# Kernel tuning notes

Hardware: AMD Instinct MI355X
Metric: run time of the kernel (lower is better)

The kernel has to match this reference:

```python
import jax, jax.numpy as jnp
import numpy as np

B, SQ, SK = 2, 2048, 2048
E = 256   # embed_dim (also per-head key dim in this MHA)
S = 256   # srcdim (also per-head value dim)
NH = 8    # num_heads
HID = 2 * S  # FFN hidden = in_dim * 2


def setup_inputs() -> dict:
    key = jax.random.key(0)
    ks = jax.random.split(key, 12)
    def w(k, shape, s=0.02):
        return jax.random.normal(k, shape, dtype=jnp.float32) * s
    return {
        "Q": jax.random.normal(ks[0], (B, SQ, E), dtype=jnp.float32),
        "H": jax.random.normal(ks[1], (B, SK, E), dtype=jnp.float32),
        "A": jax.random.normal(ks[2], (B, SK, S), dtype=jnp.float32),
        # MHA params (torch Linear convention: y = x @ W.T + b)
        "wq": w(ks[3], (NH * E, E)), "bq": jnp.zeros((NH * E,), jnp.float32),
        "wk": w(ks[4], (NH * E, E)), "bk": jnp.zeros((NH * E,), jnp.float32),
        "wv": w(ks[5], (NH * S, S)), "bv": jnp.zeros((NH * S,), jnp.float32),
        "wo": w(ks[6], (S, NH * S)), "bo": jnp.zeros((S,), jnp.float32),
        # Attension scale (Parameter(torch.ones(1)))
        "attn_scale": jnp.ones((), jnp.float32),
        # shared LayerNormA params
        "ln_g": jnp.ones((S,), jnp.float32), "ln_b": jnp.zeros((S,), jnp.float32),
        # FFN params
        "w1": w(ks[7], (HID, S)), "b1": jnp.zeros((HID,), jnp.float32),
        "w2": w(ks[8], (S, HID)), "b2": jnp.zeros((S,), jnp.float32),
    }


def _layernorm(x, g, b, eps=1e-5):
    m = x.mean(-1, keepdims=True)
    v = ((x - m) ** 2).mean(-1, keepdims=True)
    return (x - m) / jnp.sqrt(v + eps) * g + b


def reference(Q, H, A, wq, bq, wk, bk, wv, bv, wo, bo,
              attn_scale, ln_g, ln_b, w1, b1, w2, b2):
    b_, sq, _ = Q.shape
    sk = H.shape[1]
    # ---- MHA branch (A_m) ----
    q = (Q @ wq.T + bq).reshape(b_, sq, NH, E).transpose(0, 2, 1, 3)  # [b,h,sq,E]
    k = (H @ wk.T + bk).reshape(b_, sk, NH, E).transpose(0, 2, 1, 3)  # [b,h,sk,E]
    v = (A @ wv.T + bv).reshape(b_, sk, NH, S).transpose(0, 2, 1, 3)  # [b,h,sk,S]
    scores = jnp.einsum('bhqe,bhke->bhqk', q, k) / jnp.sqrt(jnp.float32(E))
    probs = jax.nn.softmax(scores, axis=-1)
    ctx = jnp.einsum('bhqk,bhkd->bhqd', probs, v)          # [b,h,sq,S]
    ctx = ctx.transpose(0, 2, 1, 3).reshape(b_, sq, NH * S)
    A_m = ctx @ wo.T + bo                                   # [b,sq,S]
    # ---- Attension branch (dot score with learned scalar scale) ----
    s2 = jnp.einsum('bqe,bke->bqk', Q, H) * attn_scale      # [b,sq,sk]
    attn_out = jax.nn.softmax(s2, axis=-1) @ A              # [b,sq,S]
    # ---- residual + LN + FFN + LN (shared LayerNormA) ----
    Ad = _layernorm(A_m + attn_out, ln_g, ln_b)
    ff = jax.nn.relu(Ad @ w1.T + b1) @ w2.T + b2
    return _layernorm(ff + Ad, ln_g, ln_b)
```

## Files before the change

kernel.cpp:

```cpp
#include <hip/hip_runtime.h>
#include <cstdint>
#include <cstddef>


typedef unsigned short u16;
typedef __attribute__((ext_vector_type(8))) short bf16x8;
typedef __attribute__((ext_vector_type(4))) short s16x4;
typedef __attribute__((ext_vector_type(4))) float f32x4;

__device__ __forceinline__ float b2f(u16 u){
  union { unsigned int i; float f; } v; v.i = ((unsigned int)u) << 16; return v.f;
}
__device__ __forceinline__ u16 f2b(float f){
  union { float f; unsigned int i; } v; v.f = f;
  unsigned int u = v.i;
  unsigned int r = (u + 0x7FFFu + ((u >> 16) & 1u)) >> 16;
  return (u16)r;
}
__device__ __forceinline__ f32x4 mfma16(bf16x8 a, bf16x8 b, f32x4 c){
  return __builtin_amdgcn_mfma_f32_16x16x32_bf16(a, b, c, 0, 0, 0);
}
__device__ __forceinline__ void gload_lds16(const void* g, void* l){
  __builtin_amdgcn_global_load_lds(
      (const __attribute__((address_space(1))) unsigned int*)g,
      (__attribute__((address_space(3))) unsigned int*)l, 16, 0, 0);
}

__global__ void detect_kernel(const u16* __restrict__ q, int* __restrict__ flag){
  __shared__ int cnt;
  if (threadIdx.x == 0) cnt = 0;
  __syncthreads();
  int c = 0;
  for (int i = threadIdx.x; i < 2048; i += 256){
    u16 u = q[i];
    int e = (u >> 7) & 0xFF;
    if (e >= 140) c++;
  }
  atomicAdd(&cnt, c);
  __syncthreads();
  if (threadIdx.x == 0) *flag = (cnt > 64) ? 1 : 0;
}

struct ConvJobs {
  const void* src[18];
  void*       dst[18];
  void*       dst2[18];
  int         n[18];
  int         mode[18];
};

__global__ void convert_all(ConvJobs J, const int* __restrict__ flag){
  const int j = blockIdx.y;
  const int n = J.n[j];
  const int mode = J.mode[j];
  const int isf = *flag;
  for (int i = blockIdx.x * blockDim.x + threadIdx.x; i < n; i += gridDim.x * blockDim.x){
    if (mode == 2){
      float f = isf ? ((const float*)J.src[j])[i] : b2f(((const u16*)J.src[j])[i]);
      ((float*)J.dst[j])[i] = f;
    } else {
      u16 hi, lo = 0;
      if (isf){
        float f = ((const float*)J.src[j])[i];
        hi = f2b(f);
        if (mode == 1) lo = f2b(f - b2f(hi));
      } else {
        hi = ((const u16*)J.src[j])[i];
      }
      ((u16*)J.dst[j])[i] = hi;
      if (mode == 1) ((u16*)J.dst2[j])[i] = lo;
    }
  }
}

template<int STORE, bool RELU>
__global__ __launch_bounds__(256) void gemm_bt(
    const u16* __restrict__ X, const u16* __restrict__ W,
    const float* __restrict__ bias, void* __restrict__ outp,
    int M, int N, int K)
{
  __shared__ __align__(16) u16 lx[128 * 64];
  __shared__ __align__(16) u16 lw[128 * 64];
  const int tid = threadIdx.x;
  const int l = tid & 63, w = tid >> 6;
  const int lg = l >> 4, lr = l & 15;
  const int wr = w >> 1, wc = w & 1;
  const int m0 = blockIdx.x * 128;
  const int n0 = blockIdx.y * 128;

  f32x4 acc[4][4];
#pragma unroll
  for (int mi = 0; mi < 4; mi++)
#pragma unroll
    for (int ni = 0; ni < 4; ni++) acc[mi][ni] = (f32x4){0.f, 0.f, 0.f, 0.f};

  const int nkt = K >> 6;
  for (int kt = 0; kt < nkt; ++kt){
    __syncthreads();
#pragma unroll
    for (int it = 0; it < 4; ++it){
      int c = it * 256 + tid;
      int row = c >> 3, j = c & 7;
      int sj = (j ^ (row & 7)) * 8;
      const u16* gx = X + (size_t)(m0 + row) * K + kt * 64 + sj;
      gload_lds16(gx, (char*)lx + c * 16);
      const u16* gw = W + (size_t)(n0 + row) * K + kt * 64 + sj;
      gload_lds16(gw, (char*)lw + c * 16);
    }
    __syncthreads();
#pragma unroll
    for (int ks = 0; ks < 2; ++ks){
      bf16x8 af[4], bfv[4];
      const int swz = ((ks * 4 + lg) ^ (lr & 7)) * 8;
#pragma unroll
      for (int mi = 0; mi < 4; mi++)
        af[mi] = *(const bf16x8*)(lx + (wr * 64 + mi * 16 + lr) * 64 + swz);
#pragma unroll
      for (int ni = 0; ni < 4; ni++)
        bfv[ni] = *(const bf16x8*)(lw + (wc * 64 + ni * 16 + lr) * 64 + swz);
#pragma unroll
      for (int mi = 0; mi < 4; mi++)
#pragma unroll
        for (int ni = 0; ni < 4; ni++)
          acc[mi][ni] = mfma16(af[mi], bfv[ni], acc[mi][ni]);
    }
  }

#pragma unroll
  for (int mi = 0; mi < 4; mi++)
#pragma unroll
    for (int ni = 0; ni < 4; ni++){
      const int gr0 = m0 + wr * 64 + mi * 16 + lg * 4;
      const int gc  = n0 + wc * 64 + ni * 16 + lr;
      const float bv = bias ? bias[gc] : 0.f;
      if (STORE == 2){
        const int b = gr0 >> 11, sk0 = gr0 & 2047;
        const int h = gc >> 8,  d   = gc & 255;
        s16x4 pk;
#pragma unroll
        for (int r = 0; r < 4; r++){
          float v = acc[mi][ni][r] + bv;
          pk[r] = (short)f2b(v);
        }
        *(s16x4*)((u16*)outp + ((size_t)((b << 3) + h) * 256 + d) * 2048 + sk0) = pk;
      } else {
#pragma unroll
        for (int r = 0; r < 4; r++){
          float v = acc[mi][ni][r] + bv;
          if (RELU) v = fmaxf(v, 0.f);
          size_t idx = (size_t)(gr0 + r) * N + gc;
          if (STORE == 0) ((u16*)outp)[idx] = f2b(v);
          else            ((float*)outp)[idx] = v;
        }
      }
    }
}

template<int STORE, bool RELU>
__global__ __launch_bounds__(256) void gemm_bt64(
    const u16* __restrict__ X, const u16* __restrict__ W,
    const float* __restrict__ bias, void* __restrict__ outp,
    int M, int N, int K)
{
  __shared__ __align__(16) u16 lx[64 * 64];
  __shared__ __align__(16) u16 lw[64 * 64];
  const int tid = threadIdx.x;
  const int l = tid & 63, w = tid >> 6;
  const int lg = l >> 4, lr = l & 15;
  const int wr = w >> 1, wc = w & 1;
  const int m0 = blockIdx.x * 64;
  const int n0 = blockIdx.y * 64;

  f32x4 acc[2][2];
#pragma unroll
  for (int mi = 0; mi < 2; mi++)
#pragma unroll
    for (int ni = 0; ni < 2; ni++) acc[mi][ni] = (f32x4){0.f, 0.f, 0.f, 0.f};

  const int nkt = K >> 6;
  for (int kt = 0; kt < nkt; ++kt){
    __syncthreads();
#pragma unroll
    for (int it = 0; it < 2; ++it){
      int c = it * 256 + tid;
      int row = c >> 3, j = c & 7;
      int sj = (j ^ (row & 7)) * 8;
      const u16* gx = X + (size_t)(m0 + row) * K + kt * 64 + sj;
      gload_lds16(gx, (char*)lx + c * 16);
      const u16* gw = W + (size_t)(n0 + row) * K + kt * 64 + sj;
      gload_lds16(gw, (char*)lw + c * 16);
    }
    __syncthreads();
#pragma unroll
    for (int ks = 0; ks < 2; ++ks){
      bf16x8 af[2], bfv[2];
      const int swz = ((ks * 4 + lg) ^ (lr & 7)) * 8;
#pragma unroll
      for (int mi = 0; mi < 2; mi++)
        af[mi] = *(const bf16x8*)(lx + (wr * 32 + mi * 16 + lr) * 64 + swz);
#pragma unroll
      for (int ni = 0; ni < 2; ni++)
        bfv[ni] = *(const bf16x8*)(lw + (wc * 32 + ni * 16 + lr) * 64 + swz);
#pragma unroll
      for (int mi = 0; mi < 2; mi++)
#pragma unroll
        for (int ni = 0; ni < 2; ni++)
          acc[mi][ni] = mfma16(af[mi], bfv[ni], acc[mi][ni]);
    }
  }

#pragma unroll
  for (int mi = 0; mi < 2; mi++)
#pragma unroll
    for (int ni = 0; ni < 2; ni++){
      const int gr0 = m0 + wr * 32 + mi * 16 + lg * 4;
      const int gc  = n0 + wc * 32 + ni * 16 + lr;
      const float bv = bias ? bias[gc] : 0.f;
#pragma unroll
      for (int r = 0; r < 4; r++){
        float v = acc[mi][ni][r] + bv;
        if (RELU) v = fmaxf(v, 0.f);
        size_t idx = (size_t)(gr0 + r) * N + gc;
        if (STORE == 0) ((u16*)outp)[idx] = f2b(v);
        else            ((float*)outp)[idx] = v;
      }
    }
}

__global__ __launch_bounds__(256) void transpose_k(const u16* __restrict__ src, u16* __restrict__ dst){
  __shared__ u16 t[64][72];
  const int b   = blockIdx.z;
  const int sk0 = blockIdx.x * 64;
  const int d0  = blockIdx.y * 64;
  const int tid = threadIdx.x;
  union U8 { bf16x8 v; u16 e[8]; };
#pragma unroll
  for (int half = 0; half < 2; ++half){
    int c = half * 256 + tid;
    int r = c >> 3, c8 = (c & 7) * 8;
    U8 u; u.v = *(const bf16x8*)(src + ((size_t)b * 2048 + sk0 + r) * 256 + d0 + c8);
#pragma unroll
    for (int i = 0; i < 8; i++) t[r][c8 + i] = u.e[i];
  }
  __syncthreads();
#pragma unroll
  for (int half = 0; half < 2; ++half){
    int c = half * 256 + tid;
    int dr = c >> 3, s8 = (c & 7) * 8;
    U8 u;
#pragma unroll
    for (int i = 0; i < 8; i++) u.e[i] = t[s8 + i][dr];
    *(bf16x8*)(dst + ((size_t)b * 256 + d0 + dr) * 2048 + sk0 + s8) = u.v;
  }
}

__global__ __launch_bounds__(256, 1) void flash_mha(
    const u16* __restrict__ Qp, const u16* __restrict__ Kp,
    const u16* __restrict__ Vt, u16* __restrict__ outp)
{
  __shared__ __align__(16) u16 bufK[64 * 256];
  __shared__ __align__(16) u16 bufV[256 * 64];
  __shared__ __align__(16) u16 ldsP[4][32 * 72];
  const int tid = threadIdx.x, l = tid & 63, w = tid >> 6;
  const int lg = l >> 4, lr = l & 15;
  const int lr7 = lr & 15 & 7;
  const int bid = blockIdx.x;
  const int xcd = bid & 7;
  const int slot = bid >> 3;
  const int by = xcd * 2 + (slot >> 4);
  const int qt = slot & 15;
  const size_t qkbase = ((size_t)(by >> 3) * 2048) * 2048 + (size_t)(by & 7) * 256;
  const size_t vbase  = (size_t)by * (256 * 2048);
  const int q0 = qt * 128 + w * 32;

  bf16x8 qf[2][8];
#pragma unroll
  for (int qb = 0; qb < 2; qb++)
#pragma unroll
    for (int ks = 0; ks < 8; ks++)
      qf[qb][ks] = *(const bf16x8*)(Qp + qkbase +
          (size_t)(q0 + qb * 16 + lr) * 2048 + ks * 32 + lg * 8);

  float mrun[2][4], lpart[2][4];
#pragma unroll
  for (int qb = 0; qb < 2; qb++)
#pragma unroll
    for (int r = 0; r < 4; r++){ mrun[qb][r] = -3e38f; lpart[qb][r] = 0.f; }
  f32x4 accO[2][16];
#pragma unroll
  for (int qb = 0; qb < 2; qb++)
#pragma unroll
    for (int db = 0; db < 16; db++) accO[qb][db] = (f32x4){0.f, 0.f, 0.f, 0.f};

  auto stageK = [&](int kv0){
#pragma unroll
    for (int it = 0; it < 8; ++it){
      int c = it * 256 + tid;
      int row = c >> 5, j = c & 31;
      const u16* g = Kp + qkbase + (size_t)(kv0 + row) * 2048 + (j ^ (row & 7)) * 8;
      gload_lds16(g, (char*)bufK + c * 16);
    }
  };
  auto stageV = [&](int kv0){
#pragma unroll
    for (int it = 0; it < 8; ++it){
      int c = it * 256 + tid;
      int row = c >> 3, j = c & 7;
      const u16* g = Vt + vbase + (size_t)row * 2048 + kv0 + (j ^ (row & 7)) * 8;
      gload_lds16(g, (char*)bufV + c * 16);
    }
  };

  stageK(0);

  for (int t = 0; t < 32; ++t){
    const int kv0 = t * 64;
    __syncthreads();
    stageV(kv0);

    f32x4 s[2][4];
#pragma unroll
    for (int qb = 0; qb < 2; qb++)
#pragma unroll
      for (int kb = 0; kb < 4; kb++) s[qb][kb] = (f32x4){0.f, 0.f, 0.f, 0.f};

    __builtin_amdgcn_s_setprio(1);
#pragma unroll
    for (int ks = 0; ks < 8; ks++){
      bf16x8 bfr[4];
      const int swz = (((ks * 4 + lg) ^ lr7)) * 8;
#pragma unroll
      for (int kb = 0; kb < 4; kb++)
        bfr[kb] = *(const bf16x8*)(bufK + (kb * 16 + lr) * 256 + swz);
#pragma unroll
      for (int qb = 0; qb < 2; qb++)
#pragma unroll
        for (int kb = 0; kb < 4; kb++)
          s[qb][kb] = mfma16(qf[qb][ks], bfr[kb], s[qb][kb]);
    }
    __builtin_amdgcn_s_setprio(0);

    float pm[2][4];
#pragma unroll
    for (int qb = 0; qb < 2; qb++){
#pragma unroll
      for (int kb = 0; kb < 4; kb++)
#pragma unroll
        for (int r = 0; r < 4; r++) s[qb][kb][r] *= 0.0625f;
#pragma unroll
      for (int r = 0; r < 4; r++)
        pm[qb][r] = fmaxf(fmaxf(s[qb][0][r], s[qb][1][r]),
                          fmaxf(s[qb][2][r], s[qb][3][r]));
#pragma unroll
      for (int m = 1; m < 16; m <<= 1)
#pragma unroll
        for (int r = 0; r < 4; r++) pm[qb][r] = fmaxf(pm[qb][r], __shfl_xor(pm[qb][r], m));
    }
    float gmax = -3e38f;
#pragma unroll
    for (int qb = 0; qb < 2; qb++)
#pragma unroll
      for (int r = 0; r < 4; r++) gmax = fmaxf(gmax, pm[qb][r] - mrun[qb][r]);
    if (__any(gmax > 8.0f)){
#pragma unroll
      for (int qb = 0; qb < 2; qb++)
#pragma unroll
        for (int r = 0; r < 4; r++){
          float mn = fmaxf(mrun[qb][r], pm[qb][r]);
          float corr = __expf(mrun[qb][r] - mn);
          mrun[qb][r] = mn;
          lpart[qb][r] *= corr;
#pragma unroll
          for (int db = 0; db < 16; db++) accO[qb][db][r] *= corr;
        }
    }
#pragma unroll
    for (int qb = 0; qb < 2; qb++)
#pragma unroll
      for (int kb = 0; kb < 4; kb++)
#pragma unroll
        for (int r = 0; r < 4; r++){
          float p = __expf(s[qb][kb][r] - mrun[qb][r]);
          lpart[qb][r] += p;
          ldsP[w][(qb * 16 + lg * 4 + r) * 72 + kb * 16 + lr] = f2b(p);
        }

    __syncthreads();
    if (t + 1 < 32) stageK(kv0 + 64);

    __builtin_amdgcn_s_setprio(1);
#pragma unroll
    for (int ks2 = 0; ks2 < 2; ++ks2){
      bf16x8 pa[2];
#pragma unroll
      for (int qb = 0; qb < 2; qb++)
        pa[qb] = *(const bf16x8*)(ldsP[w] + (qb * 16 + lr) * 72 + ks2 * 32 + lg * 8);
      const int swz = (((ks2 * 4 + lg) ^ lr7)) * 8;
#pragma unroll
      for (int db = 0; db < 16; ++db){
        bf16x8 vb = *(const bf16x8*)(bufV + (db * 16 + lr) * 64 + swz);
        accO[0][db] = mfma16(pa[0], vb, accO[0][db]);
        accO[1][db] = mfma16(pa[1], vb, accO[1][db]);
      }
    }
    __builtin_amdgcn_s_setprio(0);
  }

#pragma unroll
  for (int qb = 0; qb < 2; qb++){
    float lrun[4];
#pragma unroll
    for (int r = 0; r < 4; r++) lrun[r] = lpart[qb][r];
#pragma unroll
    for (int m = 1; m < 16; m <<= 1)
#pragma unroll
      for (int r = 0; r < 4; r++) lrun[r] += __shfl_xor(lrun[r], m);
    float inv[4];
#pragma unroll
    for (int r = 0; r < 4; r++) inv[r] = 1.f / lrun[r];
#pragma unroll
    for (int db = 0; db < 16; db++)
#pragma unroll
      for (int r = 0; r < 4; r++){
        float v = accO[qb][db][r] * inv[r];
        int q = q0 + qb * 16 + lg * 4 + r;
        int d = db * 16 + lr;
        outp[((size_t)(by >> 3) * 2048 + q) * 2048 + (size_t)(by & 7) * 256 + d] = f2b(v);
      }
  }
}

__global__ __launch_bounds__(256) void flash_b2(
    const u16* __restrict__ Qh, const u16* __restrict__ Ql,
    const u16* __restrict__ Kh, const u16* __restrict__ Kl,
    const u16* __restrict__ Vt,
    float* __restrict__ Opart, float* __restrict__ mlp,
    const float* __restrict__ p_scale, const int* __restrict__ flagp)
{
  __shared__ __align__(16) u16 bufK[64 * 256];
  __shared__ __align__(16) u16 bufV[256 * 64];
  __shared__ __align__(16) u16 ldsP[4][16 * 72];
  const int tid = threadIdx.x, l = tid & 63, w = tid >> 6;
  const int lg = l >> 4, lr = l & 15;
  const int lr7 = lr & 7;
  const int by = blockIdx.y, qt = blockIdx.x, kc = blockIdx.z;
  const size_t qkbase = (size_t)by * (2048 * 256);
  const size_t vbase  = (size_t)by * (256 * 2048);
  const float scale = *p_scale;
  const int split = *flagp;
  const int kvbase = kc * 256;
  const int q0 = qt * 64 + w * 16;

  bf16x8 qf[8], qfl[8];
#pragma unroll
  for (int ks = 0; ks < 8; ks++)
    qf[ks] = *(const bf16x8*)(Qh + qkbase + (size_t)(q0 + lr) * 256 + ks * 32 + lg * 8);
  if (split){
#pragma unroll
    for (int ks = 0; ks < 8; ks++)
      qfl[ks] = *(const bf16x8*)(Ql + qkbase + (size_t)(q0 + lr) * 256 + ks * 32 + lg * 8);
  } else {
#pragma unroll
    for (int ks = 0; ks < 8; ks++) qfl[ks] = qf[ks];
  }

  float mrun[4], lpart[4];
#pragma unroll
  for (int r = 0; r < 4; r++){ mrun[r] = -3e38f; lpart[r] = 0.f; }
  f32x4 accO[16];
#pragma unroll
  for (int db = 0; db < 16; db++) accO[db] = (f32x4){0.f, 0.f, 0.f, 0.f};

  auto stageK = [&](const u16* __restrict__ src, int kv0){
#pragma unroll
    for (int it = 0; it < 8; ++it){
      int c = it * 256 + tid;
      int row = c >> 5, j = c & 31;
      const u16* g = src + qkbase + (size_t)(kv0 + row) * 256 + (j ^ (row & 7)) * 8;
      gload_lds16(g, (char*)bufK + c * 16);
    }
  };
  auto stageV = [&](int kv0){
#pragma unroll
    for (int it = 0; it < 8; ++it){
      int c = it * 256 + tid;
      int row = c >> 3, j = c & 7;
      const u16* g = Vt + vbase + (size_t)row * 2048 + kv0 + (j ^ (row & 7)) * 8;
      gload_lds16(g, (char*)bufV + c * 16);
    }
  };

  for (int t = 0; t < 4; ++t){
    const int kv0 = kvbase + t * 64;
    __syncthreads();
    stageK(Kh, kv0);
    stageV(kv0);
    __syncthreads();

    f32x4 s[4];
#pragma unroll
    for (int kb = 0; kb < 4; kb++) s[kb] = (f32x4){0.f, 0.f, 0.f, 0.f};
#pragma unroll
    for (int ks = 0; ks < 8; ks++){
      bf16x8 bfr[4];
      const int swz = (((ks * 4 + lg) ^ lr7)) * 8;
#pragma unroll
      for (int kb = 0; kb < 4; kb++)
        bfr[kb] = *(const bf16x8*)(bufK + (kb * 16 + lr) * 256 + swz);
#pragma unroll
      for (int kb = 0; kb < 4; kb++) s[kb] = mfma16(qf[ks], bfr[kb], s[kb]);
      if (split){
#pragma unroll
        for (int kb = 0; kb < 4; kb++) s[kb] = mfma16(qfl[ks], bfr[kb], s[kb]);
      }
    }
    if (split){
      __syncthreads();
      stageK(Kl, kv0);
      __syncthreads();
#pragma unroll
      for (int ks = 0; ks < 8; ks++){
        bf16x8 bfr[4];
        const int swz = (((ks * 4 + lg) ^ lr7)) * 8;
#pragma unroll
        for (int kb = 0; kb < 4; kb++)
          bfr[kb] = *(const bf16x8*)(bufK + (kb * 16 + lr) * 256 + swz);
#pragma unroll
        for (int kb = 0; kb < 4; kb++) s[kb] = mfma16(qf[ks], bfr[kb], s[kb]);
      }
    }

#pragma unroll
    for (int kb = 0; kb < 4; kb++)
#pragma unroll
      for (int r = 0; r < 4; r++) s[kb][r] *= scale;

    float pm[4];
#pragma unroll
    for (int r = 0; r < 4; r++)
      pm[r] = fmaxf(fmaxf(s[0][r], s[1][r]), fmaxf(s[2][r], s[3][r]));
#pragma unroll
    for (int m = 1; m < 16; m <<= 1)
#pragma unroll
      for (int r = 0; r < 4; r++) pm[r] = fmaxf(pm[r], __shfl_xor(pm[r], m));

    float g = fmaxf(fmaxf(pm[0] - mrun[0], pm[1] - mrun[1]),
                    fmaxf(pm[2] - mrun[2], pm[3] - mrun[3]));
    if (__any(g > 8.0f)){
#pragma unroll
      for (int r = 0; r < 4; r++){
        float mn = fmaxf(mrun[r], pm[r]);
        float corr = __expf(mrun[r] - mn);
        mrun[r] = mn;
        lpart[r] *= corr;
#pragma unroll
        for (int db = 0; db < 16; db++) accO[db][r] *= corr;
      }
    }
#pragma unroll
    for (int kb = 0; kb < 4; kb++)
#pragma unroll
      for (int r = 0; r < 4; r++){
        float p = __expf(s[kb][r] - mrun[r]);
        lpart[r] += p;
        ldsP[w][(lg * 4 + r) * 72 + kb * 16 + lr] = f2b(p);
      }

#pragma unroll
    for (int ks2 = 0; ks2 < 2; ++ks2){
      bf16x8 pa = *(const bf16x8*)(ldsP[w] + lr * 72 + ks2 * 32 + lg * 8);
      const int swz = (((ks2 * 4 + lg) ^ lr7)) * 8;
#pragma unroll
      for (int db = 0; db < 16; ++db){
        bf16x8 vb = *(const bf16x8*)(bufV + (db * 16 + lr) * 64 + swz);
        accO[db] = mfma16(pa, vb, accO[db]);
      }
    }
  }

  float lrun[4];
#pragma unroll
  for (int r = 0; r < 4; r++) lrun[r] = lpart[r];
#pragma unroll
  for (int m = 1; m < 16; m <<= 1)
#pragma unroll
    for (int r = 0; r < 4; r++) lrun[r] += __shfl_xor(lrun[r], m);

#pragma unroll
  for (int db = 0; db < 16; db++)
#pragma unroll
    for (int r = 0; r < 4; r++){
      int q = q0 + lg * 4 + r;
      int d = db * 16 + lr;
      Opart[((size_t)((kc * 2 + by) * 2048 + q)) * 256 + d] = accO[db][r];
    }
  if (lr == 0){
#pragma unroll
    for (int r = 0; r < 4; r++){
      int idx = (kc * 2 + by) * 2048 + q0 + lg * 4 + r;
      mlp[idx] = mrun[r];
      mlp[32768 + idx] = lrun[r];
    }
  }
}

__global__ __launch_bounds__(256) void merge_k(
    const float* __restrict__ Opart, const float* __restrict__ ml,
    float* __restrict__ outp)
{
  const int w = threadIdx.x >> 6, l = threadIdx.x & 63;
  const int row = blockIdx.x * 4 + w;
  const int b = row >> 11, q = row & 2047;
  float m[8], li[8], M = -3e38f;
#pragma unroll
  for (int kc = 0; kc < 8; kc++){
    int idx = (kc * 2 + b) * 2048 + q;
    m[kc] = ml[idx];
    li[kc] = ml[32768 + idx];
    M = fmaxf(M, m[kc]);
  }
  float L = 0.f, wgt[8];
#pragma unroll
  for (int kc = 0; kc < 8; kc++){ wgt[kc] = __expf(m[kc] - M); L += li[kc] * wgt[kc]; }
  const float invL = 1.f / L;
  f32x4 o = (f32x4){0.f, 0.f, 0.f, 0.f};
#pragma unroll
  for (int kc = 0; kc < 8; kc++){
    f32x4 v = *(const f32x4*)(Opart + ((size_t)((kc * 2 + b) * 2048 + q)) * 256 + l * 4);
#pragma unroll
    for (int i = 0; i < 4; i++) o[i] += v[i] * wgt[kc];
  }
#pragma unroll
  for (int i = 0; i < 4; i++) o[i] *= invL;
  *(f32x4*)(outp + (size_t)row * 256 + l * 4) = o;
}

template<int RESF32, int OUTFLAG>
__global__ __launch_bounds__(256) void ln_k(
    const float* __restrict__ x, const void* __restrict__ res,
    const float* __restrict__ g, const float* __restrict__ bb,
    void* __restrict__ outp, const int* __restrict__ flagp)
{
  const int w = threadIdx.x >> 6, l = threadIdx.x & 63;
  const int row = blockIdx.x * 4 + w;
  const size_t off = (size_t)row * 256 + l * 4;
  f32x4 xv = *(const f32x4*)(x + off);
  float v[4];
  if (RESF32){
    f32x4 rv = *(const f32x4*)((const float*)res + off);
#pragma unroll
    for (int i = 0; i < 4; i++) v[i] = xv[i] + rv[i];
  } else {
    const u16* rp = (const u16*)res + off;
#pragma unroll
    for (int i = 0; i < 4; i++) v[i] = xv[i] + b2f(rp[i]);
  }
  float s = 0.f, sq = 0.f;
#pragma unroll
  for (int i = 0; i < 4; i++){ s += v[i]; sq += v[i] * v[i]; }
  for (int m = 1; m < 64; m <<= 1){ s += __shfl_xor(s, m); sq += __shfl_xor(sq, m); }
  const float mean = s * (1.f / 256.f);
  const float var = sq * (1.f / 256.f) - mean * mean;
  const float rstd = rsqrtf(var + 1e-5f);
  float y[4];
#pragma unroll
  for (int i = 0; i < 4; i++) y[i] = (v[i] - mean) * rstd * g[l * 4 + i] + bb[l * 4 + i];
  const bool f32out = OUTFLAG && (*flagp);
  if (f32out){
    f32x4 o;
#pragma unroll
    for (int i = 0; i < 4; i++) o[i] = y[i];
    *(f32x4*)((float*)outp + off) = o;
  } else {
    s16x4 o;
#pragma unroll
    for (int i = 0; i < 4; i++) o[i] = (short)f2b(y[i]);
    *(s16x4*)((u16*)outp + off) = o;
  }
}

extern "C" void kernel_launch(void* const* d_in, const int* in_sizes, int n_in,
                              void* d_out, int out_size, void* d_ws, size_t ws_size,
                              hipStream_t stream)
{
  (void)in_sizes; (void)n_in; (void)out_size; (void)ws_size;
  char* ws = (char*)d_ws;
  size_t off = 0;
  auto alloc = [&](size_t bytes) -> char* {
    char* p = ws + off;
    off += (bytes + 255) & ~(size_t)255;
    return p;
  };
  int*   flag    = (int*)  alloc(4);
  float* p_scale = (float*)alloc(4);
  float* p_bq    = (float*)alloc(2048 * 4);
  float* p_bk    = (float*)alloc(2048 * 4);
  float* p_bv    = (float*)alloc(2048 * 4);
  float* p_bo    = (float*)alloc(256 * 4);
  float* p_b1    = (float*)alloc(512 * 4);
  float* p_b2    = (float*)alloc(256 * 4);
  float* p_g     = (float*)alloc(256 * 4);
  float* p_b     = (float*)alloc(256 * 4);
  u16* Qc  = (u16*)alloc((size_t)1048576 * 2);
  u16* Qlo = (u16*)alloc((size_t)1048576 * 2);
  u16* Hc  = (u16*)alloc((size_t)1048576 * 2);
  u16* Hlo = (u16*)alloc((size_t)1048576 * 2);
  u16* Ac  = (u16*)alloc((size_t)1048576 * 2);
  u16* wqc = (u16*)alloc((size_t)524288 * 2);
  u16* wkc = (u16*)alloc((size_t)524288 * 2);
  u16* wvc = (u16*)alloc((size_t)524288 * 2);
  u16* woc = (u16*)alloc((size_t)524288 * 2);
  u16* w1c = (u16*)alloc((size_t)131072 * 2);
  u16* w2c = (u16*)alloc((size_t)131072 * 2);
  u16* qbuf = (u16*)alloc((size_t)4096 * 2048 * 2);
  u16* kbuf = (u16*)alloc((size_t)4096 * 2048 * 2);
  u16* vtb  = (u16*)alloc((size_t)4096 * 2048 * 2);
  u16* ctx  = (u16*)alloc((size_t)4096 * 2048 * 2);
  u16* At   = (u16*)alloc((size_t)1048576 * 2);
  float* attn_o = (float*)alloc((size_t)4096 * 256 * 4);
  float* Am     = (float*)alloc((size_t)4096 * 256 * 4);
  u16* Ad  = (u16*)alloc((size_t)1048576 * 2);
  u16* h1  = (u16*)alloc((size_t)4096 * 512 * 2);
  float* ffb = (float*)alloc((size_t)4096 * 256 * 4);

  detect_kernel<<<1, 256, 0, stream>>>((const u16*)d_in[0], flag);

  ConvJobs J{};
  auto setj = [&](int i, const void* s, void* d, void* d2, int n, int m){
    J.src[i] = s; J.dst[i] = d; J.dst2[i] = d2; J.n[i] = n; J.mode[i] = m;
  };
  setj(0,  d_in[0],  Qc,  Qlo, 1048576, 1);
  setj(1,  d_in[1],  Hc,  Hlo, 1048576, 1);
  setj(2,  d_in[2],  Ac,  nullptr, 1048576, 0);
  setj(3,  d_in[3],  wqc, nullptr, 524288, 0);
  setj(4,  d_in[5],  wkc, nullptr, 524288, 0);
  setj(5,  d_in[7],  wvc, nullptr, 524288, 0);
  setj(6,  d_in[9],  woc, nullptr, 524288, 0);
  setj(7,  d_in[14], w1c, nullptr, 131072, 0);
  setj(8,  d_in[16], w2c, nullptr, 131072, 0);
  setj(9,  d_in[4],  p_bq, nullptr, 2048, 2);
  setj(10, d_in[6],  p_bk, nullptr, 2048, 2);
  setj(11, d_in[8],  p_bv, nullptr, 2048, 2);
  setj(12, d_in[10], p_bo, nullptr, 256, 2);
  setj(13, d_in[15], p_b1, nullptr, 512, 2);
  setj(14, d_in[17], p_b2, nullptr, 256, 2);
  setj(15, d_in[12], p_g,  nullptr, 256, 2);
  setj(16, d_in[13], p_b,  nullptr, 256, 2);
  setj(17, d_in[11], p_scale, nullptr, 1, 2);
  convert_all<<<dim3(64, 18), 256, 0, stream>>>(J, flag);

  gemm_bt<0, false><<<dim3(32, 16), 256, 0, stream>>>(Qc, wqc, p_bq, qbuf, 4096, 2048, 256);
  gemm_bt<0, false><<<dim3(32, 16), 256, 0, stream>>>(Hc, wkc, p_bk, kbuf, 4096, 2048, 256);
  gemm_bt<2, false><<<dim3(32, 16), 256, 0, stream>>>(Ac, wvc, p_bv, vtb,  4096, 2048, 256);
  transpose_k<<<dim3(32, 4, 2), 256, 0, stream>>>(Ac, At);

  flash_mha<<<dim3(256), 256, 0, stream>>>(qbuf, kbuf, vtb, ctx);

  float* Opart = (float*)qbuf;
  float* mlbuf = (float*)vtb;
  flash_b2<<<dim3(32, 2, 8), 256, 0, stream>>>(Qc, Qlo, Hc, Hlo, At,
                                               Opart, mlbuf, p_scale, flag);
  merge_k<<<1024, 256, 0, stream>>>(Opart, mlbuf, attn_o);

  gemm_bt64<1, false><<<dim3(64, 4), 256, 0, stream>>>(ctx, woc, p_bo, Am, 4096, 256, 2048);
  ln_k<1, 0><<<1024, 256, 0, stream>>>(Am, attn_o, p_g, p_b, Ad, flag);
  gemm_bt64<0, true ><<<dim3(64, 8), 256, 0, stream>>>(Ad, w1c, p_b1, h1, 4096, 512, 256);
  gemm_bt64<1, false><<<dim3(64, 4), 256, 0, stream>>>(h1, w2c, p_b2, ffb, 4096, 256, 512);
  ln_k<0, 1><<<1024, 256, 0, stream>>>(ffb, Ad, p_g, p_b, d_out, flag);
}
```

Baseline: 311.5 us.

## Split flash_mha work over 8 waves with 16 query rows each

Changes the MHA flash kernel from 4 waves of 32 query rows to 8 waves of 16 query rows per block (512 threads), halving per-wave accumulator and Q-fragment registers. K/V staging is spread over twice as many threads and the per-wave P scratch is resized. The aim is more waves in flight to hide LDS and memory latency. The cost is that each V fragment loaded from LDS now feeds one MFMA instead of two, which doubles LDS read traffic per unit of compute.

```diff
diff --git a/kernel.cpp b/kernel.cpp
--- a/kernel.cpp
+++ b/kernel.cpp
@@ -254,16 +254,16 @@
   }
 }
 
-__global__ __launch_bounds__(256, 1) void flash_mha(
+__global__ __launch_bounds__(512, 2) void flash_mha(
     const u16* __restrict__ Qp, const u16* __restrict__ Kp,
     const u16* __restrict__ Vt, u16* __restrict__ outp)
 {
   __shared__ __align__(16) u16 bufK[64 * 256];
   __shared__ __align__(16) u16 bufV[256 * 64];
-  __shared__ __align__(16) u16 ldsP[4][32 * 72];
+  __shared__ __align__(16) u16 ldsP[8][16 * 72];
   const int tid = threadIdx.x, l = tid & 63, w = tid >> 6;
   const int lg = l >> 4, lr = l & 15;
-  const int lr7 = lr & 15 & 7;
+  const int lr7 = lr & 7;
   const int bid = blockIdx.x;
   const int xcd = bid & 7;
   const int slot = bid >> 3;
@@ -271,31 +271,25 @@
   const int qt = slot & 15;
   const size_t qkbase = ((size_t)(by >> 3) * 2048) * 2048 + (size_t)(by & 7) * 256;
   const size_t vbase  = (size_t)by * (256 * 2048);
-  const int q0 = qt * 128 + w * 32;
-
-  bf16x8 qf[2][8];
-#pragma unroll
-  for (int qb = 0; qb < 2; qb++)
-#pragma unroll
-    for (int ks = 0; ks < 8; ks++)
-      qf[qb][ks] = *(const bf16x8*)(Qp + qkbase +
-          (size_t)(q0 + qb * 16 + lr) * 2048 + ks * 32 + lg * 8);
-
-  float mrun[2][4], lpart[2][4];
-#pragma unroll
-  for (int qb = 0; qb < 2; qb++)
-#pragma unroll
-    for (int r = 0; r < 4; r++){ mrun[qb][r] = -3e38f; lpart[qb][r] = 0.f; }
-  f32x4 accO[2][16];
-#pragma unroll
-  for (int qb = 0; qb < 2; qb++)
-#pragma unroll
-    for (int db = 0; db < 16; db++) accO[qb][db] = (f32x4){0.f, 0.f, 0.f, 0.f};
+  const int q0 = qt * 128 + w * 16;
+
+  bf16x8 qf[8];
+#pragma unroll
+  for (int ks = 0; ks < 8; ks++)
+    qf[ks] = *(const bf16x8*)(Qp + qkbase +
+        (size_t)(q0 + lr) * 2048 + ks * 32 + lg * 8);
+
+  float mrun[4], lpart[4];
+#pragma unroll
+  for (int r = 0; r < 4; r++){ mrun[r] = -3e38f; lpart[r] = 0.f; }
+  f32x4 accO[16];
+#pragma unroll
+  for (int db = 0; db < 16; db++) accO[db] = (f32x4){0.f, 0.f, 0.f, 0.f};
 
   auto stageK = [&](int kv0){
 #pragma unroll
-    for (int it = 0; it < 8; ++it){
-      int c = it * 256 + tid;
+    for (int it = 0; it < 4; ++it){
+      int c = it * 512 + tid;
       int row = c >> 5, j = c & 31;
       const u16* g = Kp + qkbase + (size_t)(kv0 + row) * 2048 + (j ^ (row & 7)) * 8;
       gload_lds16(g, (char*)bufK + c * 16);
@@ -303,8 +297,8 @@
   };
   auto stageV = [&](int kv0){
 #pragma unroll
-    for (int it = 0; it < 8; ++it){
-      int c = it * 256 + tid;
+    for (int it = 0; it < 4; ++it){
+      int c = it * 512 + tid;
       int row = c >> 3, j = c & 7;
       const u16* g = Vt + vbase + (size_t)row * 2048 + kv0 + (j ^ (row & 7)) * 8;
       gload_lds16(g, (char*)bufV + c * 16);
@@ -318,11 +312,9 @@
     __syncthreads();
     stageV(kv0);
 
-    f32x4 s[2][4];
-#pragma unroll
-    for (int qb = 0; qb < 2; qb++)
-#pragma unroll
-      for (int kb = 0; kb < 4; kb++) s[qb][kb] = (f32x4){0.f, 0.f, 0.f, 0.f};
+    f32x4 s[4];
+#pragma unroll
+    for (int kb = 0; kb < 4; kb++) s[kb] = (f32x4){0.f, 0.f, 0.f, 0.f};
 
     __builtin_amdgcn_s_setprio(1);
 #pragma unroll
@@ -333,57 +325,45 @@
       for (int kb = 0; kb < 4; kb++)
         bfr[kb] = *(const bf16x8*)(bufK + (kb * 16 + lr) * 256 + swz);
 #pragma unroll
-      for (int qb = 0; qb < 2; qb++)
-#pragma unroll
-        for (int kb = 0; kb < 4; kb++)
-          s[qb][kb] = mfma16(qf[qb][ks], bfr[kb], s[qb][kb]);
+      for (int kb = 0; kb < 4; kb++)
+        s[kb] = mfma16(qf[ks], bfr[kb], s[kb]);
     }
     __builtin_amdgcn_s_setprio(0);
 
-    float pm[2][4];
-#pragma unroll
-    for (int qb = 0; qb < 2; qb++){
-#pragma unroll
-      for (int kb = 0; kb < 4; kb++)
-#pragma unroll
-        for (int r = 0; r < 4; r++) s[qb][kb][r] *= 0.0625f;
-#pragma unroll
-      for (int r = 0; r < 4; r++)
-        pm[qb][r] = fmaxf(fmaxf(s[qb][0][r], s[qb][1][r]),
-                          fmaxf(s[qb][2][r], s[qb][3][r]));
-#pragma unroll
-      for (int m = 1; m < 16; m <<= 1)
-#pragma unroll
-        for (int r = 0; r < 4; r++) pm[qb][r] = fmaxf(pm[qb][r], __shfl_xor(pm[qb][r], m));
-    }
-    float gmax = -3e38f;
-#pragma unroll
-    for (int qb = 0; qb < 2; qb++)
-#pragma unroll
-      for (int r = 0; r < 4; r++) gmax = fmaxf(gmax, pm[qb][r] - mrun[qb][r]);
+    float pm[4];
+#pragma unroll
+    for (int kb = 0; kb < 4; kb++)
+#pragma unroll
+      for (int r = 0; r < 4; r++) s[kb][r] *= 0.0625f;
+#pragma unroll
+    for (int r = 0; r < 4; r++)
+      pm[r] = fmaxf(fmaxf(s[0][r], s[1][r]), fmaxf(s[2][r], s[3][r]));
+#pragma unroll
+    for (int m = 1; m < 16; m <<= 1)
+#pragma unroll
+      for (int r = 0; r < 4; r++) pm[r] = fmaxf(pm[r], __shfl_xor(pm[r], m));
+
+    float gmax = fmaxf(fmaxf(pm[0] - mrun[0], pm[1] - mrun[1]),
+                       fmaxf(pm[2] - mrun[2], pm[3] - mrun[3]));
     if (__any(gmax > 8.0f)){
 #pragma unroll
-      for (int qb = 0; qb < 2; qb++)
-#pragma unroll
-        for (int r = 0; r < 4; r++){
-          float mn = fmaxf(mrun[qb][r], pm[qb][r]);
-          float corr = __expf(mrun[qb][r] - mn);
-          mrun[qb][r] = mn;
-          lpart[qb][r] *= corr;
-#pragma unroll
-          for (int db = 0; db < 16; db++) accO[qb][db][r] *= corr;
-        }
-    }
-#pragma unroll
-    for (int qb = 0; qb < 2; qb++)
-#pragma unroll
-      for (int kb = 0; kb < 4; kb++)
-#pragma unroll
-        for (int r = 0; r < 4; r++){
-          float p = __expf(s[qb][kb][r] - mrun[qb][r]);
-          lpart[qb][r] += p;
-          ldsP[w][(qb * 16 + lg * 4 + r) * 72 + kb * 16 + lr] = f2b(p);
-        }
+      for (int r = 0; r < 4; r++){
+        float mn = fmaxf(mrun[r], pm[r]);
+        float corr = __expf(mrun[r] - mn);
+        mrun[r] = mn;
+        lpart[r] *= corr;
+#pragma unroll
+        for (int db = 0; db < 16; db++) accO[db][r] *= corr;
+      }
+    }
+#pragma unroll
+    for (int kb = 0; kb < 4; kb++)
+#pragma unroll
+      for (int r = 0; r < 4; r++){
+        float p = __expf(s[kb][r] - mrun[r]);
+        lpart[r] += p;
+        ldsP[w][(lg * 4 + r) * 72 + kb * 16 + lr] = f2b(p);
+      }
 
     __syncthreads();
     if (t + 1 < 32) stageK(kv0 + 64);
@@ -391,43 +371,36 @@
     __builtin_amdgcn_s_setprio(1);
 #pragma unroll
     for (int ks2 = 0; ks2 < 2; ++ks2){
-      bf16x8 pa[2];
-#pragma unroll
-      for (int qb = 0; qb < 2; qb++)
-        pa[qb] = *(const bf16x8*)(ldsP[w] + (qb * 16 + lr) * 72 + ks2 * 32 + lg * 8);
+      bf16x8 pa = *(const bf16x8*)(ldsP[w] + lr * 72 + ks2 * 32 + lg * 8);
       const int swz = (((ks2 * 4 + lg) ^ lr7)) * 8;
 #pragma unroll
       for (int db = 0; db < 16; ++db){
         bf16x8 vb = *(const bf16x8*)(bufV + (db * 16 + lr) * 64 + swz);
-        accO[0][db] = mfma16(pa[0], vb, accO[0][db]);
-        accO[1][db] = mfma16(pa[1], vb, accO[1][db]);
+        accO[db] = mfma16(pa, vb, accO[db]);
       }
     }
     __builtin_amdgcn_s_setprio(0);
   }
 
-#pragma unroll
-  for (int qb = 0; qb < 2; qb++){
-    float lrun[4];
-#pragma unroll
-    for (int r = 0; r < 4; r++) lrun[r] = lpart[qb][r];
-#pragma unroll
-    for (int m = 1; m < 16; m <<= 1)
-#pragma unroll
-      for (int r = 0; r < 4; r++) lrun[r] += __shfl_xor(lrun[r], m);
-    float inv[4];
-#pragma unroll
-    for (int r = 0; r < 4; r++) inv[r] = 1.f / lrun[r];
-#pragma unroll
-    for (int db = 0; db < 16; db++)
-#pragma unroll
-      for (int r = 0; r < 4; r++){
-        float v = accO[qb][db][r] * inv[r];
-        int q = q0 + qb * 16 + lg * 4 + r;
-        int d = db * 16 + lr;
-        outp[((size_t)(by >> 3) * 2048 + q) * 2048 + (size_t)(by & 7) * 256 + d] = f2b(v);
-      }
-  }
+  float lrun[4];
+#pragma unroll
+  for (int r = 0; r < 4; r++) lrun[r] = lpart[r];
+#pragma unroll
+  for (int m = 1; m < 16; m <<= 1)
+#pragma unroll
+    for (int r = 0; r < 4; r++) lrun[r] += __shfl_xor(lrun[r], m);
+  float inv[4];
+#pragma unroll
+  for (int r = 0; r < 4; r++) inv[r] = 1.f / lrun[r];
+#pragma unroll
+  for (int db = 0; db < 16; db++)
+#pragma unroll
+    for (int r = 0; r < 4; r++){
+      float v = accO[db][r] * inv[r];
+      int q = q0 + lg * 4 + r;
+      int d = db * 16 + lr;
+      outp[((size_t)(by >> 3) * 2048 + q) * 2048 + (size_t)(by & 7) * 256 + d] = f2b(v);
+    }
 }
 
 __global__ __launch_bounds__(256) void flash_b2(
@@ -754,7 +727,7 @@
   gemm_bt<2, false><<<dim3(32, 16), 256, 0, stream>>>(Ac, wvc, p_bv, vtb,  4096, 2048, 256);
   transpose_k<<<dim3(32, 4, 2), 256, 0, stream>>>(Ac, At);
 
-  flash_mha<<<dim3(256), 256, 0, stream>>>(qbuf, kbuf, vtb, ctx);
+  flash_mha<<<dim3(256), 512, 0, stream>>>(qbuf, kbuf, vtb, ctx);
 
   float* Opart = (float*)qbuf;
   float* mlbuf = (float*)vtb;
```

After: 291.6 us. 6.4% less time.

## Split MHA flash attention over two KV halves with a separate merge kernel

Applied to the files above, without the earlier changes.

Each flash_mha block now runs 8 waves over 256 queries and only half of the keys and values, a split-KV scheme. Each half writes its unnormalised bf16 output plus per-row max and sum. A new merge_mha kernel rescales the two halves and combines them into ctx. The aim is more resident waves and more latency hiding per CU. The cost is extra global traffic and an extra launch. The second partial output and its stats reuse memory starting at attn_o, which only fits if later allocations are laid out contiguously. The 512-thread, 2-blocks-per-CU launch bound may also force register spills of the 128-float accumulator.

```diff
diff --git a/kernel.cpp b/kernel.cpp
--- a/kernel.cpp
+++ b/kernel.cpp
@@ -254,24 +254,28 @@
   }
 }
 
-__global__ __launch_bounds__(256, 1) void flash_mha(
+__global__ __launch_bounds__(512, 2) void flash_mha(
     const u16* __restrict__ Qp, const u16* __restrict__ Kp,
-    const u16* __restrict__ Vt, u16* __restrict__ outp)
+    const u16* __restrict__ Vt,
+    u16* __restrict__ O0, u16* __restrict__ O1, float* __restrict__ mlb)
 {
   __shared__ __align__(16) u16 bufK[64 * 256];
   __shared__ __align__(16) u16 bufV[256 * 64];
-  __shared__ __align__(16) u16 ldsP[4][32 * 72];
+  __shared__ __align__(16) u16 ldsP[8][32 * 72];
   const int tid = threadIdx.x, l = tid & 63, w = tid >> 6;
   const int lg = l >> 4, lr = l & 15;
-  const int lr7 = lr & 15 & 7;
+  const int lr7 = lr & 7;
   const int bid = blockIdx.x;
   const int xcd = bid & 7;
   const int slot = bid >> 3;
   const int by = xcd * 2 + (slot >> 4);
-  const int qt = slot & 15;
+  const int sub = slot & 15;
+  const int qt = sub >> 1;
+  const int kvc = sub & 1;
   const size_t qkbase = ((size_t)(by >> 3) * 2048) * 2048 + (size_t)(by & 7) * 256;
   const size_t vbase  = (size_t)by * (256 * 2048);
-  const int q0 = qt * 128 + w * 32;
+  const int q0 = qt * 256 + w * 32;
+  const int kvbase = kvc * 1024;
 
   bf16x8 qf[2][8];
 #pragma unroll
@@ -294,8 +298,8 @@
 
   auto stageK = [&](int kv0){
 #pragma unroll
-    for (int it = 0; it < 8; ++it){
-      int c = it * 256 + tid;
+    for (int it = 0; it < 4; ++it){
+      int c = it * 512 + tid;
       int row = c >> 5, j = c & 31;
       const u16* g = Kp + qkbase + (size_t)(kv0 + row) * 2048 + (j ^ (row & 7)) * 8;
       gload_lds16(g, (char*)bufK + c * 16);
@@ -303,18 +307,18 @@
   };
   auto stageV = [&](int kv0){
 #pragma unroll
-    for (int it = 0; it < 8; ++it){
-      int c = it * 256 + tid;
+    for (int it = 0; it < 4; ++it){
+      int c = it * 512 + tid;
       int row = c >> 3, j = c & 7;
       const u16* g = Vt + vbase + (size_t)row * 2048 + kv0 + (j ^ (row & 7)) * 8;
       gload_lds16(g, (char*)bufV + c * 16);
     }
   };
 
-  stageK(0);
-
-  for (int t = 0; t < 32; ++t){
-    const int kv0 = t * 64;
+  stageK(kvbase);
+
+  for (int t = 0; t < 16; ++t){
+    const int kv0 = kvbase + t * 64;
     __syncthreads();
     stageV(kv0);
 
@@ -386,7 +390,7 @@
         }
 
     __syncthreads();
-    if (t + 1 < 32) stageK(kv0 + 64);
+    if (t + 1 < 16) stageK(kv0 + 64);
 
     __builtin_amdgcn_s_setprio(1);
 #pragma unroll
@@ -406,6 +410,7 @@
     __builtin_amdgcn_s_setprio(0);
   }
 
+  u16* Op = kvc ? O1 : O0;
 #pragma unroll
   for (int qb = 0; qb < 2; qb++){
     float lrun[4];
@@ -415,19 +420,50 @@
     for (int m = 1; m < 16; m <<= 1)
 #pragma unroll
       for (int r = 0; r < 4; r++) lrun[r] += __shfl_xor(lrun[r], m);
-    float inv[4];
-#pragma unroll
-    for (int r = 0; r < 4; r++) inv[r] = 1.f / lrun[r];
 #pragma unroll
     for (int db = 0; db < 16; db++)
 #pragma unroll
       for (int r = 0; r < 4; r++){
-        float v = accO[qb][db][r] * inv[r];
         int q = q0 + qb * 16 + lg * 4 + r;
         int d = db * 16 + lr;
-        outp[((size_t)(by >> 3) * 2048 + q) * 2048 + (size_t)(by & 7) * 256 + d] = f2b(v);
-      }
-  }
+        Op[((size_t)(by >> 3) * 2048 + q) * 2048 + (size_t)(by & 7) * 256 + d] =
+            f2b(accO[qb][db][r]);
+      }
+    if (lr == 0){
+#pragma unroll
+      for (int r = 0; r < 4; r++){
+        int idx = kvc * 32768 + by * 2048 + q0 + qb * 16 + lg * 4 + r;
+        mlb[idx] = mrun[qb][r];
+        mlb[65536 + idx] = lrun[r];
+      }
+    }
+  }
+}
+
+__global__ __launch_bounds__(256) void merge_mha(
+    u16* __restrict__ O0, const u16* __restrict__ O1,
+    const float* __restrict__ mlb)
+{
+  const size_t i8 = (size_t)blockIdx.x * 256 + threadIdx.x;
+  const size_t i = i8 * 8;
+  const int row = (int)(i >> 11);
+  const int col = (int)(i & 2047);
+  const int by = ((row >> 11) << 3) + (col >> 8);
+  const int byq = by * 2048 + (row & 2047);
+  const float m0 = mlb[byq],          l0 = mlb[65536 + byq];
+  const float m1 = mlb[32768 + byq],  l1 = mlb[98304 + byq];
+  const float M = fmaxf(m0, m1);
+  float w0 = __expf(m0 - M), w1 = __expf(m1 - M);
+  const float invL = 1.f / (l0 * w0 + l1 * w1);
+  w0 *= invL; w1 *= invL;
+  union U8 { bf16x8 v; u16 e[8]; };
+  U8 a, b, o;
+  a.v = *(const bf16x8*)(O0 + i);
+  b.v = *(const bf16x8*)(O1 + i);
+#pragma unroll
+  for (int j = 0; j < 8; j++)
+    o.e[j] = f2b(b2f(a.e[j]) * w0 + b2f(b.e[j]) * w1);
+  *(bf16x8*)(O0 + i) = o.v;
 }
 
 __global__ __launch_bounds__(256) void flash_b2(
@@ -723,6 +759,9 @@
   u16* h1  = (u16*)alloc((size_t)4096 * 512 * 2);
   float* ffb = (float*)alloc((size_t)4096 * 256 * 4);
 
+  u16*   O1  = (u16*)attn_o;
+  float* mlb = (float*)((char*)attn_o + (size_t)4096 * 2048 * 2);
+
   detect_kernel<<<1, 256, 0, stream>>>((const u16*)d_in[0], flag);
 
   ConvJobs J{};
@@ -754,7 +793,8 @@
   gemm_bt<2, false><<<dim3(32, 16), 256, 0, stream>>>(Ac, wvc, p_bv, vtb,  4096, 2048, 256);
   transpose_k<<<dim3(32, 4, 2), 256, 0, stream>>>(Ac, At);
 
-  flash_mha<<<dim3(256), 256, 0, stream>>>(qbuf, kbuf, vtb, ctx);
+  flash_mha<<<dim3(256), 512, 0, stream>>>(qbuf, kbuf, vtb, ctx, O1, mlb);
+  merge_mha<<<dim3(4096), 256, 0, stream>>>(ctx, O1, mlb);
 
   float* Opart = (float*)qbuf;
   float* mlbuf = (float*)vtb;
```

Result: slower. 346.2 us (+11.1%).
